# Kernel optimization log

Hardware: AMD Instinct MI355X
Metric: run time of the kernel (lower is better)

## Reference

```python
import jax, jax.numpy as jnp
import numpy as np

N_NODES = 100000
N_EDGES = 600000
D = 128
HEADS = 8
REL = 9
N_GRAPHS = 64


def _relconv(h, coeff, basis, w_loop, b, src, dst, etypes, n_nodes):
    # DGL RelGraphConv, basis regularizer (num_bases == num_rels), sum aggregation,
    # self-loop, bias, relu activation (dropout inactive at eval).
    W = jnp.einsum('rb,bio->rio', coeff, basis)  # [REL, D, D]
    hsrc = h[src]                                # [E, D] gather
    msg = jnp.zeros((hsrc.shape[0], W.shape[2]), h.dtype)
    for r in range(REL):  # small fixed relation set
        msg = msg + jnp.where((etypes == r)[:, None], hsrc @ W[r], 0.0)
    agg = jax.ops.segment_sum(msg, dst, num_segments=n_nodes)
    return jax.nn.relu(agg + h @ w_loop + b)


def _graph_norm(x, seg, n_graphs, w, b, ms):
    # scatter-based per-subgraph normalization (graphNorm)
    counts = jax.ops.segment_sum(jnp.ones((x.shape[0],), x.dtype), seg, num_segments=n_graphs)[:, None]
    mean = jax.ops.segment_sum(x, seg, num_segments=n_graphs) / counts
    sub = x - mean[seg] * ms
    var = jax.ops.segment_sum(sub * sub, seg, num_segments=n_graphs) / counts
    std = jnp.sqrt(var + 1e-6)
    return w * sub / std[seg] + b


def _layer_norm(x, g, b):
    mu = x.mean(-1, keepdims=True)
    v = jnp.mean((x - mu) ** 2, -1, keepdims=True)
    return g * (x - mu) / jnp.sqrt(v + 1e-5) + b


def _forward(h, src, dst, etypes, seg, num_graphs,
             q_coeff, q_basis, q_loop, q_bias,
             k_coeff, k_basis, k_loop, k_bias,
             v_coeff, v_basis, v_loop, v_bias,
             o_w, o_b, gn1_w, gn1_b, gn1_ms, ln1_g, ln1_b,
             gn2_w, gn2_b, gn2_ms, ffn1_w, ffn1_b, ffn2_w, ffn2_b,
             ln2_g, ln2_b):
    n = h.shape[0]
    hn = _graph_norm(h, seg, num_graphs, gn1_w, gn1_b, gn1_ms)
    Q = _relconv(hn, q_coeff, q_basis, q_loop, q_bias, src, dst, etypes, n)
    K = _relconv(hn, k_coeff, k_basis, k_loop, k_bias, src, dst, etypes, n)
    V = _relconv(hn, v_coeff, v_basis, v_loop, v_bias, src, dst, etypes, n)
    dh = D // HEADS
    Qh = Q.reshape(n, HEADS, dh)
    Kh = K.reshape(n, HEADS, dh)
    Vh = V.reshape(n, HEADS, dh)
    # edge dot-product attention: score_e = <K[src], Q[dst]> per head
    score = (Kh[src] * Qh[dst]).sum(-1, keepdims=True)            # [E, H, 1]
    score = jnp.exp(jnp.clip(score / np.float32(np.sqrt(dh)), -10.0, 10.0))
    wV = jax.ops.segment_sum(Vh[src] * score, dst, num_segments=n)  # [N, H, dh]
    z = jax.ops.segment_sum(score, dst, num_segments=n)             # [N, H, 1]
    attn = (wV / (z + 1e-6)).reshape(n, D)
    hO = attn @ o_w + o_b
    h1 = _layer_norm(hO, ln1_g, ln1_b)
    h2 = _graph_norm(h1, seg, num_graphs, gn2_w, gn2_b, gn2_ms)
    h3 = jax.nn.relu(h2 @ ffn1_w + ffn1_b) @ ffn2_w + ffn2_b
    return _layer_norm(h3, ln2_g, ln2_b)


def setup_inputs() -> dict:
    key = jax.random.key(0)
    ks = jax.random.split(key, 32)
    s = np.float32(1.0 / np.sqrt(D))
    inp = {
        'h': jax.random.normal(ks[0], (N_NODES, D), jnp.float32),
        'src': jax.random.randint(ks[1], (N_EDGES,), 0, N_NODES),
        'dst': jax.random.randint(ks[2], (N_EDGES,), 0, N_NODES),
        'etypes': jax.random.randint(ks[3], (N_EDGES,), 0, REL),
        'seg': jnp.sort(jax.random.randint(ks[4], (N_NODES,), 0, N_GRAPHS)),
        'num_graphs': N_GRAPHS,
    }
    def lin(k, i, o):
        return jax.random.normal(k, (i, o), jnp.float32) / np.float32(np.sqrt(i))
    for idx, nm in enumerate(['q', 'k', 'v']):
        base = 5 + idx * 4
        inp[nm + '_coeff'] = jax.random.normal(ks[base], (REL, REL), jnp.float32) / np.float32(np.sqrt(REL))
        inp[nm + '_basis'] = jax.random.normal(ks[base + 1], (REL, D, D), jnp.float32) * s
        inp[nm + '_loop'] = lin(ks[base + 2], D, D)
        inp[nm + '_bias'] = jnp.zeros((D,), jnp.float32)
    inp['o_w'] = lin(ks[17], D, D)
    inp['o_b'] = jnp.zeros((D,), jnp.float32)
    for nm in ['gn1', 'gn2']:
        inp[nm + '_w'] = jnp.ones((D,), jnp.float32)
        inp[nm + '_b'] = jnp.zeros((D,), jnp.float32)
        inp[nm + '_ms'] = jnp.ones((D,), jnp.float32)
    inp['ln1_g'] = jnp.ones((D,), jnp.float32)
    inp['ln1_b'] = jnp.zeros((D,), jnp.float32)
    inp['ln2_g'] = jnp.ones((D,), jnp.float32)
    inp['ln2_b'] = jnp.zeros((D,), jnp.float32)
    inp['ffn1_w'] = lin(ks[18], D, 2 * D)
    inp['ffn1_b'] = jnp.zeros((2 * D,), jnp.float32)
    inp['ffn2_w'] = lin(ks[19], 2 * D, D)
    inp['ffn2_b'] = jnp.zeros((D,), jnp.float32)
    return inp


def reference(h, src, dst, etypes, seg, num_graphs,
              q_coeff, q_basis, q_loop, q_bias,
              k_coeff, k_basis, k_loop, k_bias,
              v_coeff, v_basis, v_loop, v_bias,
              o_w, o_b, gn1_w, gn1_b, gn1_ms, ln1_g, ln1_b,
              gn2_w, gn2_b, gn2_ms, ffn1_w, ffn1_b, ffn2_w, ffn2_b,
              ln2_g, ln2_b):
    return _forward(h, src, dst, etypes, seg, num_graphs,
                    q_coeff, q_basis, q_loop, q_bias,
                    k_coeff, k_basis, k_loop, k_bias,
                    v_coeff, v_basis, v_loop, v_bias,
                    o_w, o_b, gn1_w, gn1_b, gn1_ms, ln1_g, ln1_b,
                    gn2_w, gn2_b, gn2_ms, ffn1_w, ffn1_b, ffn2_w, ffn2_b,
                    ln2_g, ln2_b)
```

## Files before the change

kernel.cpp:

```cpp
#include <hip/hip_runtime.h>
#include <math.h>

#define N_NODES 100000
#define N_EDGES 600000
#define D 128
#define REL 9
#define NG 64

typedef float f32x4 __attribute__((ext_vector_type(4)));
typedef _Float16 f16x8 __attribute__((ext_vector_type(8)));

__device__ __forceinline__ ushort f2h(float x) {
    union { _Float16 h; ushort u; } c; c.h = (_Float16)x; return c.u;
}
__device__ __forceinline__ float h2f(ushort u) {
    union { ushort u; _Float16 h; } c; c.u = u; return (float)c.h;
}

__device__ __forceinline__ void ld16(const ushort* g, ushort* l) {
    __builtin_amdgcn_global_load_lds(
        (const __attribute__((address_space(1))) unsigned int*)g,
        (__attribute__((address_space(3))) unsigned int*)l, 16, 0, 0);
}

__device__ __forceinline__ int lbound(const int* __restrict__ a, int n, int key) {
    int lo = 0, hi = n;
    while (lo < hi) { int mid = (lo + hi) >> 1; if (a[mid] < key) lo = mid + 1; else hi = mid; }
    return lo;
}

__global__ void hist_kernel(const int* __restrict__ dst, int* __restrict__ cnt) {
    int e = blockIdx.x * 256 + threadIdx.x;
    if (e < N_EDGES) atomicAdd(&cnt[dst[e]], 1);
}

__global__ void scan1_kernel(const int* __restrict__ cnt, int* __restrict__ excl,
                             int* __restrict__ bsum, int n) {
    __shared__ int s[1024];
    int tid = threadIdx.x;
    int i = blockIdx.x * 1024 + tid;
    int v = (i < n) ? cnt[i] : 0;
    s[tid] = v;
    __syncthreads();
    for (int off = 1; off < 1024; off <<= 1) {
        int t = (tid >= off) ? s[tid - off] : 0;
        __syncthreads();
        s[tid] += t;
        __syncthreads();
    }
    if (i < n) excl[i] = s[tid] - v;
    if (tid == 1023) bsum[blockIdx.x] = s[1023];
}

__global__ void scan2_kernel(int* __restrict__ bsum, int nb) {
    __shared__ int s[128];
    int tid = threadIdx.x;
    int v = (tid < nb) ? bsum[tid] : 0;
    s[tid] = v;
    __syncthreads();
    for (int off = 1; off < 128; off <<= 1) {
        int t = (tid >= off) ? s[tid - off] : 0;
        __syncthreads();
        s[tid] += t;
        __syncthreads();
    }
    if (tid < nb) bsum[tid] = s[tid] - v;
}

__global__ void scan3_kernel(int* __restrict__ excl, const int* __restrict__ bsum, int n) {
    int i = blockIdx.x * 1024 + threadIdx.x;
    if (i < n) excl[i] += bsum[blockIdx.x];
}

__global__ void scatter_kernel(const int* __restrict__ src, const int* __restrict__ dst,
                               const int* __restrict__ ety, const int* __restrict__ estart,
                               int* __restrict__ cur, int* __restrict__ ssrc,
                               int* __restrict__ setp) {
    int e = blockIdx.x * 256 + threadIdx.x;
    if (e < N_EDGES) {
        int d = dst[e];
        int pos = estart[d] + atomicAdd(&cur[d], 1);
        ssrc[pos] = src[e];
        setp[pos] = ety[e];
    }
}

__global__ __launch_bounds__(256)
void gn_stats(const float* __restrict__ x, const int* __restrict__ seg,
              float* __restrict__ gsum, float* __restrict__ gsumsq) {
    int ch = threadIdx.x & 127;
    int rr = threadIdx.x >> 7;
    int n0 = blockIdx.x * 128;
    int nend = min(n0 + 128, N_NODES);
    float sx = 0.f, sxx = 0.f;
    int cg = -1;
    for (int n = n0 + rr; n < nend; n += 2) {
        int g = seg[n];
        if (g != cg) {
            if (cg >= 0) { atomicAdd(&gsum[cg * D + ch], sx); atomicAdd(&gsumsq[cg * D + ch], sxx); }
            cg = g; sx = 0.f; sxx = 0.f;
        }
        float v = x[(size_t)n * D + ch];
        sx += v; sxx += v * v;
    }
    if (cg >= 0) { atomicAdd(&gsum[cg * D + ch], sx); atomicAdd(&gsumsq[cg * D + ch], sxx); }
}

__global__ void gn_final(const float* __restrict__ gsum, const float* __restrict__ gsumsq,
                         const int* __restrict__ seg, const float* __restrict__ w,
                         const float* __restrict__ b, const float* __restrict__ ms,
                         float* __restrict__ sc, float* __restrict__ off) {
    int g = blockIdx.x, ch = threadIdx.x;
    int lo = lbound(seg, N_NODES, g), hi = lbound(seg, N_NODES, g + 1);
    float cnt = (float)max(hi - lo, 1);
    float mean = gsum[g * D + ch] / cnt;
    float mm = mean * ms[ch];
    float var = gsumsq[g * D + ch] / cnt - 2.f * mm * mean + mm * mm;
    float rstd = rsqrtf(var + 1e-6f);
    float s = w[ch] * rstd;
    sc[g * D + ch] = s;
    off[g * D + ch] = b[ch] - s * mm;
}

__global__ __launch_bounds__(256)
void gn_apply(const float* __restrict__ x, const int* __restrict__ seg,
              const float* __restrict__ sc, const float* __restrict__ off,
              ushort* __restrict__ outhf) {
    int t = blockIdx.x * 256 + threadIdx.x;
    int n = t >> 6;
    if (n >= N_NODES) return;
    int ch = (t & 63) * 2;
    int g = seg[n];
    float2 xv = *(const float2*)&x[(size_t)n * D + ch];
    float2 s2 = *(const float2*)&sc[g * D + ch];
    float2 o2 = *(const float2*)&off[g * D + ch];
    ushort2 o;
    o.x = f2h(s2.x * xv.x + o2.x);
    o.y = f2h(s2.y * xv.y + o2.y);
    *(ushort2*)&outhf[(size_t)n * D + ch] = o;
}

__global__ void build_bt_qkv(const float* __restrict__ coeff, const float* __restrict__ basis,
                             const float* __restrict__ loop_w, const float* __restrict__ bias_in,
                             ushort* __restrict__ Bt, float* __restrict__ bias_out) {
    int t = blockIdx.x * 256 + threadIdx.x;
    if (t < 128) bias_out[t] = bias_in[t];
    if (t >= 128 * 1280) return;
    int o = t / 1280;
    int k = t - o * 1280;
    float v;
    if (k < 128) {
        v = loop_w[k * 128 + o];
    } else {
        int kk = k - 128;
        int r = kk >> 7, i = kk & 127;
        v = 0.f;
#pragma unroll
        for (int b = 0; b < REL; ++b)
            v += coeff[r * REL + b] * basis[((size_t)b * 128 + i) * 128 + o];
    }
    Bt[(size_t)o * 1280 + k] = f2h(v);
}

__global__ void transpose_cast(const float* __restrict__ W, int I, int O, ushort* __restrict__ Bt) {
    int t = blockIdx.x * 256 + threadIdx.x;
    if (t >= I * O) return;
    int n = t / I, k = t - n * I;
    Bt[(size_t)n * I + k] = f2h(W[(size_t)k * O + n]);
}

__global__ __launch_bounds__(256)
void s_pass(const ushort* __restrict__ hnhf, const int* __restrict__ ssrc,
            const int* __restrict__ setp, const int* __restrict__ estart,
            const int* __restrict__ ecnt, ushort* __restrict__ Ab, int c0, int c1) {
    int n = c0 + ((blockIdx.x * 256 + threadIdx.x) >> 6);
    if (n >= c1) return;
    int lane = threadIdx.x & 63;
    int e0 = estart[n], e1 = e0 + ecnt[n];
    float ax0=0,ay0=0,ax1=0,ay1=0,ax2=0,ay2=0,ax3=0,ay3=0,ax4=0,ay4=0;
    float ax5=0,ay5=0,ax6=0,ay6=0,ax7=0,ay7=0,ax8=0,ay8=0;
    for (int e = e0; e < e1; ++e) {
        int s = ssrc[e];
        int r = __builtin_amdgcn_readfirstlane(setp[e]);
        ushort2 hv = *(const ushort2*)&hnhf[(size_t)s * D + 2 * lane];
        float vx = h2f(hv.x), vy = h2f(hv.y);
        switch (r) {
            case 0: ax0 += vx; ay0 += vy; break;
            case 1: ax1 += vx; ay1 += vy; break;
            case 2: ax2 += vx; ay2 += vy; break;
            case 3: ax3 += vx; ay3 += vy; break;
            case 4: ax4 += vx; ay4 += vy; break;
            case 5: ax5 += vx; ay5 += vy; break;
            case 6: ax6 += vx; ay6 += vy; break;
            case 7: ax7 += vx; ay7 += vy; break;
            default: ax8 += vx; ay8 += vy; break;
        }
    }
    ushort* arow = Ab + (size_t)(n - c0) * 1280;
    *(ushort2*)&arow[2 * lane] = *(const ushort2*)&hnhf[(size_t)n * D + 2 * lane];
    ushort2 t;
#define ST(r) t.x = f2h(ax##r); t.y = f2h(ay##r); *(ushort2*)&arow[128 + r * 128 + 2 * lane] = t;
    ST(0) ST(1) ST(2) ST(3) ST(4) ST(5) ST(6) ST(7) ST(8)
#undef ST
}

template<bool RELU, bool F16OUT>
__global__ __launch_bounds__(256, 3)
void mfma_gemm(const ushort* __restrict__ A, int lda, int M,
               const ushort* __restrict__ Bt, int K,
               const float* __restrict__ bias, void* __restrict__ Cout, int ldc) {
    __shared__ ushort As[128 * 64];
    __shared__ ushort Bs[128 * 64];
    const int tid = threadIdx.x;
    const int lane = tid & 63;
    const int wave = tid >> 6;
    const int wm = wave & 1, wn = wave >> 1;
    const int quad = lane >> 4, l16 = lane & 15;
    const int col0 = blockIdx.x * 128, row0 = blockIdx.y * 128;

    const ushort* sA[4];
    const ushort* sB[4];
#pragma unroll
    for (int i = 0; i < 4; ++i) {
        int rs = (wave * 4 + i) * 8 + (lane >> 3);
        int slot = lane & 7;
        int kg = slot ^ (rs & 7);
        int ra = row0 + rs; if (ra >= M) ra = M - 1;
        sA[i] = A + (size_t)ra * lda + kg * 8;
        sB[i] = Bt + (size_t)(col0 + rs) * K + kg * 8;
    }

    f32x4 acc[4][4];
#pragma unroll
    for (int i = 0; i < 4; ++i)
#pragma unroll
        for (int j = 0; j < 4; ++j) acc[i][j] = (f32x4){0.f, 0.f, 0.f, 0.f};

    for (int kc = 0; kc < K; kc += 64) {
#pragma unroll
        for (int i = 0; i < 4; ++i) {
            ld16(sA[i] + kc, &As[(wave * 4 + i) * 512]);
            ld16(sB[i] + kc, &Bs[(wave * 4 + i) * 512]);
        }
        __syncthreads();
#pragma unroll
        for (int h = 0; h < 2; ++h) {
            f16x8 af[4], bf[4];
#pragma unroll
            for (int i = 0; i < 4; ++i) {
                int r = wm * 64 + i * 16 + l16;
                af[i] = *(const f16x8*)&As[r * 64 + (((h * 4 + quad) ^ (r & 7)) * 8)];
                int c = wn * 64 + i * 16 + l16;
                bf[i] = *(const f16x8*)&Bs[c * 64 + (((h * 4 + quad) ^ (c & 7)) * 8)];
            }
#pragma unroll
            for (int i = 0; i < 4; ++i)
#pragma unroll
                for (int j = 0; j < 4; ++j)
                    acc[i][j] = __builtin_amdgcn_mfma_f32_16x16x32_f16(af[i], bf[j], acc[i][j], 0, 0, 0);
        }
        __syncthreads();
    }

#pragma unroll
    for (int i = 0; i < 4; ++i) {
        int gr0 = row0 + wm * 64 + i * 16 + quad * 4;
#pragma unroll
        for (int r = 0; r < 4; ++r) {
            int grow = gr0 + r;
            if (grow >= M) continue;
#pragma unroll
            for (int j = 0; j < 4; ++j) {
                int gcol = col0 + wn * 64 + j * 16 + l16;
                float v = acc[i][j][r] + bias[gcol];
                if (RELU) v = fmaxf(v, 0.f);
                if (F16OUT) ((ushort*)Cout)[(size_t)grow * ldc + gcol] = f2h(v);
                else        ((float*)Cout)[(size_t)grow * ldc + gcol] = v;
            }
        }
    }
}

__global__ __launch_bounds__(256)
void attn_kernel(const ushort* __restrict__ C, const int* __restrict__ ssrc,
                 const int* __restrict__ estart, const int* __restrict__ ecnt,
                 ushort* __restrict__ attnhf) {
    int n = (blockIdx.x * 256 + threadIdx.x) >> 6;
    if (n >= N_NODES) return;
    int lane = threadIdx.x & 63;
    ushort2 qh = *(const ushort2*)&C[(size_t)n * 384 + 2 * lane];
    float qx = h2f(qh.x), qy = h2f(qh.y);
    int e0 = estart[n], e1 = e0 + ecnt[n];
    float wvx = 0.f, wvy = 0.f, z = 0.f;
    int e = e0;
    for (; e + 2 <= e1; e += 2) {
        int s0 = ssrc[e], s1 = ssrc[e + 1];
        ushort2 k0 = *(const ushort2*)&C[(size_t)s0 * 384 + 128 + 2 * lane];
        ushort2 k1 = *(const ushort2*)&C[(size_t)s1 * 384 + 128 + 2 * lane];
        ushort2 v0 = *(const ushort2*)&C[(size_t)s0 * 384 + 256 + 2 * lane];
        ushort2 v1 = *(const ushort2*)&C[(size_t)s1 * 384 + 256 + 2 * lane];
        float d0 = h2f(k0.x) * qx + h2f(k0.y) * qy;
        float d1 = h2f(k1.x) * qx + h2f(k1.y) * qy;
        d0 += __shfl_xor(d0, 1); d1 += __shfl_xor(d1, 1);
        d0 += __shfl_xor(d0, 2); d1 += __shfl_xor(d1, 2);
        d0 += __shfl_xor(d0, 4); d1 += __shfl_xor(d1, 4);
        float sc0 = __expf(fminf(fmaxf(d0 * 0.25f, -10.f), 10.f));
        float sc1 = __expf(fminf(fmaxf(d1 * 0.25f, -10.f), 10.f));
        wvx += sc0 * h2f(v0.x) + sc1 * h2f(v1.x);
        wvy += sc0 * h2f(v0.y) + sc1 * h2f(v1.y);
        z += sc0 + sc1;
    }
    if (e < e1) {
        int s = ssrc[e];
        ushort2 kh = *(const ushort2*)&C[(size_t)s * 384 + 128 + 2 * lane];
        float d = h2f(kh.x) * qx + h2f(kh.y) * qy;
        d += __shfl_xor(d, 1);
        d += __shfl_xor(d, 2);
        d += __shfl_xor(d, 4);
        float sc = __expf(fminf(fmaxf(d * 0.25f, -10.f), 10.f));
        ushort2 vh = *(const ushort2*)&C[(size_t)s * 384 + 256 + 2 * lane];
        wvx += sc * h2f(vh.x); wvy += sc * h2f(vh.y); z += sc;
    }
    float inv = 1.f / (z + 1e-6f);
    ushort2 o;
    o.x = f2h(wvx * inv);
    o.y = f2h(wvy * inv);
    *(ushort2*)&attnhf[(size_t)n * D + 2 * lane] = o;
}

__global__ __launch_bounds__(256)
void ln_kernel(const float* __restrict__ x, const float* __restrict__ g,
               const float* __restrict__ b, float* __restrict__ out) {
    int n = (blockIdx.x * 256 + threadIdx.x) >> 6;
    if (n >= N_NODES) return;
    int lane = threadIdx.x & 63;
    float2 v = ((const float2*)&x[(size_t)n * D])[lane];
    float s = v.x + v.y;
#pragma unroll
    for (int off = 1; off < 64; off <<= 1) s += __shfl_xor(s, off);
    float mu = s * (1.f / 128.f);
    float dx = v.x - mu, dy = v.y - mu;
    float vs = dx * dx + dy * dy;
#pragma unroll
    for (int off = 1; off < 64; off <<= 1) vs += __shfl_xor(vs, off);
    float rstd = rsqrtf(vs * (1.f / 128.f) + 1e-5f);
    float2 gg = ((const float2*)g)[lane];
    float2 bb = ((const float2*)b)[lane];
    ((float2*)&out[(size_t)n * D])[lane] =
        make_float2(gg.x * dx * rstd + bb.x, gg.y * dy * rstd + bb.y);
}

extern "C" void kernel_launch(void* const* d_in, const int* in_sizes, int n_in,
                              void* d_out, int out_size, void* d_ws, size_t ws_size,
                              hipStream_t stream) {
    (void)in_sizes; (void)n_in; (void)out_size;
    const float* h     = (const float*)d_in[0];
    const int*   src   = (const int*)d_in[1];
    const int*   dst   = (const int*)d_in[2];
    const int*   ety   = (const int*)d_in[3];
    const int*   seg   = (const int*)d_in[4];
    const float* coeffs[3] = {(const float*)d_in[6],  (const float*)d_in[10], (const float*)d_in[14]};
    const float* bases [3] = {(const float*)d_in[7],  (const float*)d_in[11], (const float*)d_in[15]};
    const float* loops [3] = {(const float*)d_in[8],  (const float*)d_in[12], (const float*)d_in[16]};
    const float* pbias [3] = {(const float*)d_in[9],  (const float*)d_in[13], (const float*)d_in[17]};
    const float* o_w   = (const float*)d_in[18];
    const float* o_b   = (const float*)d_in[19];
    const float* gn1_w = (const float*)d_in[20];
    const float* gn1_b = (const float*)d_in[21];
    const float* gn1_ms= (const float*)d_in[22];
    const float* gn2_w = (const float*)d_in[23];
    const float* gn2_b = (const float*)d_in[24];
    const float* gn2_ms= (const float*)d_in[25];
    const float* ln1_g = (const float*)d_in[26];
    const float* ln1_b = (const float*)d_in[27];
    const float* ln2_g = (const float*)d_in[28];
    const float* ln2_b = (const float*)d_in[29];
    const float* ffn1_w= (const float*)d_in[30];
    const float* ffn1_b= (const float*)d_in[31];
    const float* ffn2_w= (const float*)d_in[32];
    const float* ffn2_b= (const float*)d_in[33];

    char* p = (char*)d_ws;
    auto take = [&](size_t bytes) { char* r = p; p += (bytes + 255) & ~(size_t)255; return r; };
    int*    ecnt   = (int*)take((size_t)N_NODES * 4);
    int*    estart = (int*)take((size_t)N_NODES * 4);
    int*    ecur   = (int*)take((size_t)N_NODES * 4);
    int*    bsum   = (int*)take(512);
    int*    ssrc   = (int*)take((size_t)N_EDGES * 4);
    int*    setp   = (int*)take((size_t)N_EDGES * 4);
    float*  gsum   = (float*)take((size_t)NG * D * 4 * 2);
    float*  gsumsq = gsum + NG * D;
    float*  gsc    = (float*)take((size_t)NG * D * 4);
    float*  goff   = (float*)take((size_t)NG * D * 4);
    ushort* Btqkv  = (ushort*)take((size_t)384 * 1280 * 2);
    float*  biasq  = (float*)take(384 * 4);
    ushort* Bto    = (ushort*)take((size_t)128 * 128 * 2);
    ushort* Btf1   = (ushort*)take((size_t)256 * 128 * 2);
    ushort* Btf2   = (ushort*)take((size_t)128 * 256 * 2);
    ushort* hnhf   = (ushort*)take((size_t)N_NODES * D * 2);
    ushort* attnhf = (ushort*)take((size_t)N_NODES * D * 2);
    ushort* Cqkv   = (ushort*)take((size_t)N_NODES * 384 * 2);
    float*  hO     = (float*)take((size_t)N_NODES * D * 4);
    size_t used = (size_t)(p - (char*)d_ws);
    size_t avail = (ws_size > used) ? ws_size - used : 0;
    int NC = 1;
    if (avail < (size_t)N_NODES * 1280 * 2) NC = 4;
    if (NC == 4 && avail < ((size_t)(N_NODES / 4 + 1) * 1280 * 2)) NC = 8;
    ushort* Ab = (ushort*)p;
    const int chunk = (N_NODES + NC - 1) / NC;

    ushort* gn2hf  = Cqkv;
    ushort* ffn1hf = (ushort*)((char*)Cqkv + 25600000);
    float*  ffn2o  = (float*)hnhf;

    const int EB = (N_EDGES + 255) / 256;
    const int SB = (N_NODES + 1023) / 1024;
    const int WB = (N_NODES * 64 + 255) / 256;
    const int GB = (N_NODES + 127) / 128;

    hipMemsetAsync(ecnt, 0, N_NODES * sizeof(int), stream);
    hipMemsetAsync(ecur, 0, N_NODES * sizeof(int), stream);
    hist_kernel<<<EB, 256, 0, stream>>>(dst, ecnt);
    scan1_kernel<<<SB, 1024, 0, stream>>>(ecnt, estart, bsum, N_NODES);
    scan2_kernel<<<1, 128, 0, stream>>>(bsum, SB);
    scan3_kernel<<<SB, 1024, 0, stream>>>(estart, bsum, N_NODES);
    scatter_kernel<<<EB, 256, 0, stream>>>(src, dst, ety, estart, ecur, ssrc, setp);

    for (int pj = 0; pj < 3; ++pj)
        build_bt_qkv<<<640, 256, 0, stream>>>(coeffs[pj], bases[pj], loops[pj], pbias[pj],
                                              Btqkv + (size_t)pj * 128 * 1280, biasq + pj * 128);
    transpose_cast<<<64, 256, 0, stream>>>(o_w, 128, 128, Bto);
    transpose_cast<<<128, 256, 0, stream>>>(ffn1_w, 128, 256, Btf1);
    transpose_cast<<<128, 256, 0, stream>>>(ffn2_w, 256, 128, Btf2);

    hipMemsetAsync(gsum, 0, (size_t)NG * D * 8, stream);
    gn_stats<<<GB, 256, 0, stream>>>(h, seg, gsum, gsumsq);
    gn_final<<<NG, 128, 0, stream>>>(gsum, gsumsq, seg, gn1_w, gn1_b, gn1_ms, gsc, goff);
    gn_apply<<<WB, 256, 0, stream>>>(h, seg, gsc, goff, hnhf);

    for (int c = 0; c < NC; ++c) {
        int c0 = c * chunk;
        int c1 = min(N_NODES, c0 + chunk);
        int rows = c1 - c0;
        if (rows <= 0) break;
        s_pass<<<(rows + 3) / 4, 256, 0, stream>>>(hnhf, ssrc, setp, estart, ecnt, Ab, c0, c1);
        mfma_gemm<true, true><<<dim3(3, (rows + 127) / 128), 256, 0, stream>>>(
            Ab, 1280, rows, Btqkv, 1280, biasq, Cqkv + (size_t)c0 * 384, 384);
    }

    attn_kernel<<<WB, 256, 0, stream>>>(Cqkv, ssrc, estart, ecnt, attnhf);

    mfma_gemm<false, false><<<dim3(1, (N_NODES + 127) / 128), 256, 0, stream>>>(
        attnhf, 128, N_NODES, Bto, 128, o_b, hO, 128);
    ln_kernel<<<WB, 256, 0, stream>>>(hO, ln1_g, ln1_b, hO);

    hipMemsetAsync(gsum, 0, (size_t)NG * D * 8, stream);
    gn_stats<<<GB, 256, 0, stream>>>(hO, seg, gsum, gsumsq);
    gn_final<<<NG, 128, 0, stream>>>(gsum, gsumsq, seg, gn2_w, gn2_b, gn2_ms, gsc, goff);
    gn_apply<<<WB, 256, 0, stream>>>(hO, seg, gsc, goff, gn2hf);

    mfma_gemm<true, true><<<dim3(2, (N_NODES + 127) / 128), 256, 0, stream>>>(
        gn2hf, 128, N_NODES, Btf1, 128, ffn1_b, ffn1hf, 256);
    mfma_gemm<false, false><<<dim3(1, (N_NODES + 127) / 128), 256, 0, stream>>>(
        ffn1hf, 256, N_NODES, Btf2, 256, ffn2_b, ffn2o, 128);

    ln_kernel<<<WB, 256, 0, stream>>>(ffn2o, ln2_g, ln2_b, (float*)d_out);
}
```

Before: 851.9 us.

## Fuse layernorm into GEMM epilogues, split QKV A operand, merge K/V attention loads

Fuses both layernorms into the epilogues of the output-projection and FFN2 GEMMs, using cross-wave row reductions through shared memory. This removes the two standalone LN passes and their fp32 round trips. The QKV GEMM now reads the self-loop features straight from hnhf through a split A pointer, so s_pass no longer copies them into the staging buffer. The post-attention activation is kept in fp16, with half-precision variants of the graph-norm kernels, which trades some precision for less memory traffic. The attention kernel has half the wave load K and half load V with ushort4 loads, then shares the dot product across the halves with a shuffle.

```diff
diff --git a/kernel.cpp b/kernel.cpp
--- a/kernel.cpp
+++ b/kernel.cpp
@@ -101,6 +101,27 @@
             cg = g; sx = 0.f; sxx = 0.f;
         }
         float v = x[(size_t)n * D + ch];
+        sx += v; sxx += v * v;
+    }
+    if (cg >= 0) { atomicAdd(&gsum[cg * D + ch], sx); atomicAdd(&gsumsq[cg * D + ch], sxx); }
+}
+
+__global__ __launch_bounds__(256)
+void gn_stats_h(const ushort* __restrict__ x, const int* __restrict__ seg,
+                float* __restrict__ gsum, float* __restrict__ gsumsq) {
+    int ch = threadIdx.x & 127;
+    int rr = threadIdx.x >> 7;
+    int n0 = blockIdx.x * 128;
+    int nend = min(n0 + 128, N_NODES);
+    float sx = 0.f, sxx = 0.f;
+    int cg = -1;
+    for (int n = n0 + rr; n < nend; n += 2) {
+        int g = seg[n];
+        if (g != cg) {
+            if (cg >= 0) { atomicAdd(&gsum[cg * D + ch], sx); atomicAdd(&gsumsq[cg * D + ch], sxx); }
+            cg = g; sx = 0.f; sxx = 0.f;
+        }
+        float v = h2f(x[(size_t)n * D + ch]);
         sx += v; sxx += v * v;
     }
     if (cg >= 0) { atomicAdd(&gsum[cg * D + ch], sx); atomicAdd(&gsumsq[cg * D + ch], sxx); }
@@ -137,6 +158,24 @@
     ushort2 o;
     o.x = f2h(s2.x * xv.x + o2.x);
     o.y = f2h(s2.y * xv.y + o2.y);
+    *(ushort2*)&outhf[(size_t)n * D + ch] = o;
+}
+
+__global__ __launch_bounds__(256)
+void gn_apply_h(const ushort* __restrict__ x, const int* __restrict__ seg,
+                const float* __restrict__ sc, const float* __restrict__ off,
+                ushort* __restrict__ outhf) {
+    int t = blockIdx.x * 256 + threadIdx.x;
+    int n = t >> 6;
+    if (n >= N_NODES) return;
+    int ch = (t & 63) * 2;
+    int g = seg[n];
+    ushort2 xv = *(const ushort2*)&x[(size_t)n * D + ch];
+    float2 s2 = *(const float2*)&sc[g * D + ch];
+    float2 o2 = *(const float2*)&off[g * D + ch];
+    ushort2 o;
+    o.x = f2h(s2.x * h2f(xv.x) + o2.x);
+    o.y = f2h(s2.y * h2f(xv.y) + o2.y);
     *(ushort2*)&outhf[(size_t)n * D + ch] = o;
 }
 
@@ -196,17 +235,16 @@
             default: ax8 += vx; ay8 += vy; break;
         }
     }
-    ushort* arow = Ab + (size_t)(n - c0) * 1280;
-    *(ushort2*)&arow[2 * lane] = *(const ushort2*)&hnhf[(size_t)n * D + 2 * lane];
+    ushort* arow = Ab + (size_t)(n - c0) * 1152;
     ushort2 t;
-#define ST(r) t.x = f2h(ax##r); t.y = f2h(ay##r); *(ushort2*)&arow[128 + r * 128 + 2 * lane] = t;
+#define ST(r) t.x = f2h(ax##r); t.y = f2h(ay##r); *(ushort2*)&arow[r * 128 + 2 * lane] = t;
     ST(0) ST(1) ST(2) ST(3) ST(4) ST(5) ST(6) ST(7) ST(8)
 #undef ST
 }
 
-template<bool RELU, bool F16OUT>
+template<bool SPLITA, bool RELU, bool F16OUT>
 __global__ __launch_bounds__(256, 3)
-void mfma_gemm(const ushort* __restrict__ A, int lda, int M,
+void mfma_gemm(const ushort* __restrict__ A1, const ushort* __restrict__ A2, int lda2, int M,
                const ushort* __restrict__ Bt, int K,
                const float* __restrict__ bias, void* __restrict__ Cout, int ldc) {
     __shared__ ushort As[128 * 64];
@@ -218,16 +256,17 @@
     const int quad = lane >> 4, l16 = lane & 15;
     const int col0 = blockIdx.x * 128, row0 = blockIdx.y * 128;
 
-    const ushort* sA[4];
+    const ushort* sA1[4];
+    const ushort* sA2[4];
     const ushort* sB[4];
 #pragma unroll
     for (int i = 0; i < 4; ++i) {
         int rs = (wave * 4 + i) * 8 + (lane >> 3);
-        int slot = lane & 7;
-        int kg = slot ^ (rs & 7);
+        int kg = (lane & 7) ^ (rs & 7);
         int ra = row0 + rs; if (ra >= M) ra = M - 1;
-        sA[i] = A + (size_t)ra * lda + kg * 8;
-        sB[i] = Bt + (size_t)(col0 + rs) * K + kg * 8;
+        sA1[i] = SPLITA ? (A1 + (size_t)ra * 128 + kg * 8) : nullptr;
+        sA2[i] = A2 + (size_t)ra * lda2 + kg * 8;
+        sB[i]  = Bt + (size_t)(col0 + rs) * K + kg * 8;
     }
 
     f32x4 acc[4][4];
@@ -239,7 +278,8 @@
     for (int kc = 0; kc < K; kc += 64) {
 #pragma unroll
         for (int i = 0; i < 4; ++i) {
-            ld16(sA[i] + kc, &As[(wave * 4 + i) * 512]);
+            const ushort* as = (SPLITA && kc < 128) ? (sA1[i] + kc) : (sA2[i] + (SPLITA ? kc - 128 : kc));
+            ld16(as, &As[(wave * 4 + i) * 512]);
             ld16(sB[i] + kc, &Bs[(wave * 4 + i) * 512]);
         }
         __syncthreads();
@@ -281,6 +321,113 @@
     }
 }
 
+template<bool F16OUT>
+__global__ __launch_bounds__(256, 3)
+void mfma_gemm_ln(const ushort* __restrict__ A, int lda, int M,
+                  const ushort* __restrict__ Bt, int K,
+                  const float* __restrict__ bias, const float* __restrict__ lng,
+                  const float* __restrict__ lnb, void* __restrict__ Cout) {
+    __shared__ ushort As[128 * 64];
+    __shared__ ushort Bs[128 * 64];
+    __shared__ float rsum[2][128];
+    __shared__ float rsq[2][128];
+    const int tid = threadIdx.x;
+    const int lane = tid & 63;
+    const int wave = tid >> 6;
+    const int wm = wave & 1, wn = wave >> 1;
+    const int quad = lane >> 4, l16 = lane & 15;
+    const int row0 = blockIdx.y * 128;
+
+    const ushort* sA[4];
+    const ushort* sB[4];
+#pragma unroll
+    for (int i = 0; i < 4; ++i) {
+        int rs = (wave * 4 + i) * 8 + (lane >> 3);
+        int kg = (lane & 7) ^ (rs & 7);
+        int ra = row0 + rs; if (ra >= M) ra = M - 1;
+        sA[i] = A + (size_t)ra * lda + kg * 8;
+        sB[i] = Bt + (size_t)rs * K + kg * 8;
+    }
+
+    f32x4 acc[4][4];
+#pragma unroll
+    for (int i = 0; i < 4; ++i)
+#pragma unroll
+        for (int j = 0; j < 4; ++j) acc[i][j] = (f32x4){0.f, 0.f, 0.f, 0.f};
+
+    for (int kc = 0; kc < K; kc += 64) {
+#pragma unroll
+        for (int i = 0; i < 4; ++i) {
+            ld16(sA[i] + kc, &As[(wave * 4 + i) * 512]);
+            ld16(sB[i] + kc, &Bs[(wave * 4 + i) * 512]);
+        }
+        __syncthreads();
+#pragma unroll
+        for (int h = 0; h < 2; ++h) {
+            f16x8 af[4], bf[4];
+#pragma unroll
+            for (int i = 0; i < 4; ++i) {
+                int r = wm * 64 + i * 16 + l16;
+                af[i] = *(const f16x8*)&As[r * 64 + (((h * 4 + quad) ^ (r & 7)) * 8)];
+                int c = wn * 64 + i * 16 + l16;
+                bf[i] = *(const f16x8*)&Bs[c * 64 + (((h * 4 + quad) ^ (c & 7)) * 8)];
+            }
+#pragma unroll
+            for (int i = 0; i < 4; ++i)
+#pragma unroll
+                for (int j = 0; j < 4; ++j)
+                    acc[i][j] = __builtin_amdgcn_mfma_f32_16x16x32_f16(af[i], bf[j], acc[i][j], 0, 0, 0);
+        }
+        __syncthreads();
+    }
+
+#pragma unroll
+    for (int i = 0; i < 4; ++i) {
+#pragma unroll
+        for (int r = 0; r < 4; ++r) {
+            float s = 0.f, q = 0.f;
+#pragma unroll
+            for (int j = 0; j < 4; ++j) {
+                float v = acc[i][j][r] + bias[wn * 64 + j * 16 + l16];
+                s += v; q += v * v;
+            }
+            s += __shfl_xor(s, 1); q += __shfl_xor(q, 1);
+            s += __shfl_xor(s, 2); q += __shfl_xor(q, 2);
+            s += __shfl_xor(s, 4); q += __shfl_xor(q, 4);
+            s += __shfl_xor(s, 8); q += __shfl_xor(q, 8);
+            if (l16 == 0) {
+                int row = wm * 64 + i * 16 + quad * 4 + r;
+                rsum[wn][row] = s;
+                rsq[wn][row] = q;
+            }
+        }
+    }
+    __syncthreads();
+
+#pragma unroll
+    for (int i = 0; i < 4; ++i) {
+#pragma unroll
+        for (int r = 0; r < 4; ++r) {
+            int row = wm * 64 + i * 16 + quad * 4 + r;
+            int grow = row0 + row;
+            if (grow >= M) continue;
+            float tot = rsum[0][row] + rsum[1][row];
+            float tq  = rsq[0][row] + rsq[1][row];
+            float mu = tot * (1.f / 128.f);
+            float var = tq * (1.f / 128.f) - mu * mu;
+            float rstd = rsqrtf(var + 1e-5f);
+#pragma unroll
+            for (int j = 0; j < 4; ++j) {
+                int gcol = wn * 64 + j * 16 + l16;
+                float v = acc[i][j][r] + bias[gcol];
+                float o = lng[gcol] * (v - mu) * rstd + lnb[gcol];
+                if (F16OUT) ((ushort*)Cout)[(size_t)grow * 128 + gcol] = f2h(o);
+                else        ((float*)Cout)[(size_t)grow * 128 + gcol] = o;
+            }
+        }
+    }
+}
+
 __global__ __launch_bounds__(256)
 void attn_kernel(const ushort* __restrict__ C, const int* __restrict__ ssrc,
                  const int* __restrict__ estart, const int* __restrict__ ecnt,
@@ -288,66 +435,50 @@
     int n = (blockIdx.x * 256 + threadIdx.x) >> 6;
     if (n >= N_NODES) return;
     int lane = threadIdx.x & 63;
-    ushort2 qh = *(const ushort2*)&C[(size_t)n * 384 + 2 * lane];
-    float qx = h2f(qh.x), qy = h2f(qh.y);
+    ushort4 qh = *(const ushort4*)&C[(size_t)n * 384 + 4 * (lane & 31)];
+    float q0 = h2f(qh.x), q1 = h2f(qh.y), q2 = h2f(qh.z), q3 = h2f(qh.w);
     int e0 = estart[n], e1 = e0 + ecnt[n];
-    float wvx = 0.f, wvy = 0.f, z = 0.f;
+    float w0 = 0.f, w1 = 0.f, w2 = 0.f, w3 = 0.f, z = 0.f;
+    const bool isK = lane < 32;
     int e = e0;
     for (; e + 2 <= e1; e += 2) {
         int s0 = ssrc[e], s1 = ssrc[e + 1];
-        ushort2 k0 = *(const ushort2*)&C[(size_t)s0 * 384 + 128 + 2 * lane];
-        ushort2 k1 = *(const ushort2*)&C[(size_t)s1 * 384 + 128 + 2 * lane];
-        ushort2 v0 = *(const ushort2*)&C[(size_t)s0 * 384 + 256 + 2 * lane];
-        ushort2 v1 = *(const ushort2*)&C[(size_t)s1 * 384 + 256 + 2 * lane];
-        float d0 = h2f(k0.x) * qx + h2f(k0.y) * qy;
-        float d1 = h2f(k1.x) * qx + h2f(k1.y) * qy;
+        ushort4 a = *(const ushort4*)&C[(size_t)s0 * 384 + 128 + 4 * lane];
+        ushort4 b = *(const ushort4*)&C[(size_t)s1 * 384 + 128 + 4 * lane];
+        float d0 = h2f(a.x) * q0 + h2f(a.y) * q1 + h2f(a.z) * q2 + h2f(a.w) * q3;
+        float d1 = h2f(b.x) * q0 + h2f(b.y) * q1 + h2f(b.z) * q2 + h2f(b.w) * q3;
         d0 += __shfl_xor(d0, 1); d1 += __shfl_xor(d1, 1);
         d0 += __shfl_xor(d0, 2); d1 += __shfl_xor(d1, 2);
-        d0 += __shfl_xor(d0, 4); d1 += __shfl_xor(d1, 4);
+        float p0 = __shfl_xor(d0, 32), p1 = __shfl_xor(d1, 32);
+        d0 = isK ? d0 : p0; d1 = isK ? d1 : p1;
         float sc0 = __expf(fminf(fmaxf(d0 * 0.25f, -10.f), 10.f));
         float sc1 = __expf(fminf(fmaxf(d1 * 0.25f, -10.f), 10.f));
-        wvx += sc0 * h2f(v0.x) + sc1 * h2f(v1.x);
-        wvy += sc0 * h2f(v0.y) + sc1 * h2f(v1.y);
+        w0 += sc0 * h2f(a.x) + sc1 * h2f(b.x);
+        w1 += sc0 * h2f(a.y) + sc1 * h2f(b.y);
+        w2 += sc0 * h2f(a.z) + sc1 * h2f(b.z);
+        w3 += sc0 * h2f(a.w) + sc1 * h2f(b.w);
         z += sc0 + sc1;
     }
     if (e < e1) {
-        int s = ssrc[e];
-        ushort2 kh = *(const ushort2*)&C[(size_t)s * 384 + 128 + 2 * lane];
-        float d = h2f(kh.x) * qx + h2f(kh.y) * qy;
-        d += __shfl_xor(d, 1);
-        d += __shfl_xor(d, 2);
-        d += __shfl_xor(d, 4);
-        float sc = __expf(fminf(fmaxf(d * 0.25f, -10.f), 10.f));
-        ushort2 vh = *(const ushort2*)&C[(size_t)s * 384 + 256 + 2 * lane];
-        wvx += sc * h2f(vh.x); wvy += sc * h2f(vh.y); z += sc;
-    }
-    float inv = 1.f / (z + 1e-6f);
-    ushort2 o;
-    o.x = f2h(wvx * inv);
-    o.y = f2h(wvy * inv);
-    *(ushort2*)&attnhf[(size_t)n * D + 2 * lane] = o;
-}
-
-__global__ __launch_bounds__(256)
-void ln_kernel(const float* __restrict__ x, const float* __restrict__ g,
-               const float* __restrict__ b, float* __restrict__ out) {
-    int n = (blockIdx.x * 256 + threadIdx.x) >> 6;
-    if (n >= N_NODES) return;
-    int lane = threadIdx.x & 63;
-    float2 v = ((const float2*)&x[(size_t)n * D])[lane];
-    float s = v.x + v.y;
-#pragma unroll
-    for (int off = 1; off < 64; off <<= 1) s += __shfl_xor(s, off);
-    float mu = s * (1.f / 128.f);
-    float dx = v.x - mu, dy = v.y - mu;
-    float vs = dx * dx + dy * dy;
-#pragma unroll
-    for (int off = 1; off < 64; off <<= 1) vs += __shfl_xor(vs, off);
-    float rstd = rsqrtf(vs * (1.f / 128.f) + 1e-5f);
-    float2 gg = ((const float2*)g)[lane];
-    float2 bb = ((const float2*)b)[lane];
-    ((float2*)&out[(size_t)n * D])[lane] =
-        make_float2(gg.x * dx * rstd + bb.x, gg.y * dy * rstd + bb.y);
+        int s0 = ssrc[e];
+        ushort4 a = *(const ushort4*)&C[(size_t)s0 * 384 + 128 + 4 * lane];
+        float d0 = h2f(a.x) * q0 + h2f(a.y) * q1 + h2f(a.z) * q2 + h2f(a.w) * q3;
+        d0 += __shfl_xor(d0, 1);
+        d0 += __shfl_xor(d0, 2);
+        float p0 = __shfl_xor(d0, 32);
+        d0 = isK ? d0 : p0;
+        float sc0 = __expf(fminf(fmaxf(d0 * 0.25f, -10.f), 10.f));
+        w0 += sc0 * h2f(a.x); w1 += sc0 * h2f(a.y);
+        w2 += sc0 * h2f(a.z); w3 += sc0 * h2f(a.w);
+        z += sc0;
+    }
+    if (!isK) {
+        float inv = 1.f / (z + 1e-6f);
+        ushort4 o;
+        o.x = f2h(w0 * inv); o.y = f2h(w1 * inv);
+        o.z = f2h(w2 * inv); o.w = f2h(w3 * inv);
+        *(ushort4*)&attnhf[(size_t)n * D + 4 * (lane - 32)] = o;
+    }
 }
 
 extern "C" void kernel_launch(void* const* d_in, const int* in_sizes, int n_in,
@@ -399,24 +530,24 @@
     ushort* Btf2   = (ushort*)take((size_t)128 * 256 * 2);
     ushort* hnhf   = (ushort*)take((size_t)N_NODES * D * 2);
     ushort* attnhf = (ushort*)take((size_t)N_NODES * D * 2);
+    ushort* h1hf   = (ushort*)take((size_t)N_NODES * D * 2);
     ushort* Cqkv   = (ushort*)take((size_t)N_NODES * 384 * 2);
-    float*  hO     = (float*)take((size_t)N_NODES * D * 4);
     size_t used = (size_t)(p - (char*)d_ws);
     size_t avail = (ws_size > used) ? ws_size - used : 0;
     int NC = 1;
-    if (avail < (size_t)N_NODES * 1280 * 2) NC = 4;
-    if (NC == 4 && avail < ((size_t)(N_NODES / 4 + 1) * 1280 * 2)) NC = 8;
+    if (avail < (size_t)N_NODES * 1152 * 2) NC = 4;
+    if (NC == 4 && avail < ((size_t)(N_NODES / 4 + 1) * 1152 * 2)) NC = 8;
     ushort* Ab = (ushort*)p;
     const int chunk = (N_NODES + NC - 1) / NC;
 
     ushort* gn2hf  = Cqkv;
     ushort* ffn1hf = (ushort*)((char*)Cqkv + 25600000);
-    float*  ffn2o  = (float*)hnhf;
 
     const int EB = (N_EDGES + 255) / 256;
     const int SB = (N_NODES + 1023) / 1024;
     const int WB = (N_NODES * 64 + 255) / 256;
     const int GB = (N_NODES + 127) / 128;
+    const int RB = (N_NODES + 127) / 128;
 
     hipMemsetAsync(ecnt, 0, N_NODES * sizeof(int), stream);
     hipMemsetAsync(ecur, 0, N_NODES * sizeof(int), stream);
@@ -444,25 +575,23 @@
         int rows = c1 - c0;
         if (rows <= 0) break;
         s_pass<<<(rows + 3) / 4, 256, 0, stream>>>(hnhf, ssrc, setp, estart, ecnt, Ab, c0, c1);
-        mfma_gemm<true, true><<<dim3(3, (rows + 127) / 128), 256, 0, stream>>>(
-            Ab, 1280, rows, Btqkv, 1280, biasq, Cqkv + (size_t)c0 * 384, 384);
+        mfma_gemm<true, true, true><<<dim3(3, (rows + 127) / 128), 256, 0, stream>>>(
+            hnhf + (size_t)c0 * 128, Ab, 1152, rows, Btqkv, 1280, biasq,
+            Cqkv + (size_t)c0 * 384, 384);
     }
 
     attn_kernel<<<WB, 256, 0, stream>>>(Cqkv, ssrc, estart, ecnt, attnhf);
 
-    mfma_gemm<false, false><<<dim3(1, (N_NODES + 127) / 128), 256, 0, stream>>>(
-        attnhf, 128, N_NODES, Bto, 128, o_b, hO, 128);
-    ln_kernel<<<WB, 256, 0, stream>>>(hO, ln1_g, ln1_b, hO);
+    mfma_gemm_ln<true><<<dim3(1, RB), 256, 0, stream>>>(
+        attnhf, 128, N_NODES, Bto, 128, o_b, ln1_g, ln1_b, h1hf);
 
     hipMemsetAsync(gsum, 0, (size_t)NG * D * 8, stream);
-    gn_stats<<<GB, 256, 0, stream>>>(hO, seg, gsum, gsumsq);
+    gn_stats_h<<<GB, 256, 0, stream>>>(h1hf, seg, gsum, gsumsq);
     gn_final<<<NG, 128, 0, stream>>>(gsum, gsumsq, seg, gn2_w, gn2_b, gn2_ms, gsc, goff);
-    gn_apply<<<WB, 256, 0, stream>>>(hO, seg, gsc, goff, gn2hf);
-
-    mfma_gemm<true, true><<<dim3(2, (N_NODES + 127) / 128), 256, 0, stream>>>(
-        gn2hf, 128, N_NODES, Btf1, 128, ffn1_b, ffn1hf, 256);
-    mfma_gemm<false, false><<<dim3(1, (N_NODES + 127) / 128), 256, 0, stream>>>(
-        ffn1hf, 256, N_NODES, Btf2, 256, ffn2_b, ffn2o, 128);
-
-    ln_kernel<<<WB, 256, 0, stream>>>(ffn2o, ln2_g, ln2_b, (float*)d_out);
-}
+    gn_apply_h<<<WB, 256, 0, stream>>>(h1hf, seg, gsc, goff, gn2hf);
+
+    mfma_gemm<false, true, true><<<dim3(2, RB), 256, 0, stream>>>(
+        nullptr, gn2hf, 128, N_NODES, Btf1, 128, ffn1_b, ffn1hf, 256);
+    mfma_gemm_ln<false><<<dim3(1, RB), 256, 0, stream>>>(
+        ffn1hf, 256, N_NODES, Btf2, 256, ffn2_b, ln2_g, ln2_b, (float*)d_out);
+}
```

Measured after the change: 803.3 us. -5.7%, faster.
